# Kernel optimization log

Hardware: AMD Instinct MI355X
Metric: run time of the kernel (lower is better)

Reference implementation:

```python
import jax, jax.numpy as jnp
import numpy as np

B, M, D = 4096, 200, 100          # batch, max_neighbor, embed_dim
NSYM, NENT = 100001, 5000         # num_symbols+1, num_entities


def setup_inputs() -> dict:
    key = jax.random.key(0)
    ks = jax.random.split(key, 12)
    s = 0.05  # weight init scale to keep activations sane
    return {
        "connections": jax.random.randint(ks[0], (B, M, 3), 0, NENT),
        "target": jax.random.randint(ks[1], (B, 1, 2), 0, NENT),
        "symbol_emb": jax.random.normal(ks[2], (NSYM, D), jnp.float32),
        "co_entities": jax.random.uniform(ks[3], (NENT, NENT), dtype=jnp.float32),
        "gcn_w_weight": jax.random.normal(ks[4], (D, 2 * D), jnp.float32) * s,
        "gcn_w_bias": jax.random.normal(ks[5], (D,), jnp.float32) * s,
        "gcn_b": jnp.zeros((D,), jnp.float32),
        "attn_w_weight": jax.random.normal(ks[6], (1, D), jnp.float32) * s,
        "attn_w_bias": jnp.zeros((1,), jnp.float32),
        "gate_w_weight": jax.random.normal(ks[7], (1, D), jnp.float32) * s,
        "gate_w_bias": jnp.zeros((1,), jnp.float32),
        "gate_b": jnp.zeros((1,), jnp.float32),
    }


def reference(connections, target, symbol_emb, co_entities,
              gcn_w_weight, gcn_w_bias, gcn_b,
              attn_w_weight, attn_w_bias,
              gate_w_weight, gate_w_bias, gate_b):
    # --- neighbor gather ---
    relations = connections[:, :, 1]            # [B, M]
    entities = connections[:, :, 2]             # [B, M]
    entself = connections[:, 0, 0]              # [B]
    rel_embeds = symbol_emb[relations]          # [B, M, D]
    ent_embeds = symbol_emb[entities]           # [B, M, D]
    entself_embeds = symbol_emb[entself]        # [B, D]

    # co-occurrence weights: co[b, m] = co_entities[entities[b,m], target_ent[b]]
    target_ent = target[:, 0, 0]                # [B]
    co_weight = co_entities[entities, target_ent[:, None]]  # [B, M]

    # --- linear + leaky_relu (gcn) ---
    concat = jnp.concatenate([rel_embeds, ent_embeds], axis=-1)   # [B, M, 2D]
    out = jnp.einsum('bmk,dk->bmd', concat, gcn_w_weight) + gcn_w_bias + gcn_b
    out = jax.nn.leaky_relu(out, negative_slope=0.01)             # [B, M, D]

    # --- attention over neighbors ---
    attn_out = jnp.einsum('bmd,od->bmo', out, attn_w_weight) + attn_w_bias  # [B, M, 1]
    attn_weight = jax.nn.softmax(attn_out, axis=1)
    out_attn = jnp.einsum('bmd,bmo->bd', out, attn_weight)        # [B, D]

    # --- sigmoid gate ---
    gate = jax.nn.sigmoid(out_attn @ gate_w_weight.T + gate_w_bias + gate_b)  # [B, 1]
    out_neigh = out_attn * gate

    # --- co-weighted neighbor aggregation ---
    neighbor_emb = jnp.einsum('bm,bmd->bd', co_weight, ent_embeds)  # [B, D]

    return out_neigh + entself_embeds * (1.0 - gate) + neighbor_emb
```

## Files before the change

### kernel.cpp

```cpp
#include <hip/hip_runtime.h>

#define BB   4096
#define MM   200
#define DD   100
#define NENT 5000
#define CH   100
#define LPW  30
#define PTW  101

typedef _Float16 f16x2 __attribute__((ext_vector_type(2)));
typedef unsigned uint2v __attribute__((ext_vector_type(2)));

#if defined(__has_builtin)
#if __has_builtin(__builtin_amdgcn_fdot2)
#define HAS_FDOT2 1
#endif
#endif

__device__ __forceinline__ f16x2 uh(unsigned u) { return __builtin_bit_cast(f16x2, u); }
__device__ __forceinline__ float2 h2f(f16x2 h) { return make_float2((float)h.x, (float)h.y); }


__global__ __launch_bounds__(256) void precompute_kernel(
    const float* __restrict__ sym, const float* __restrict__ W,
    const float* __restrict__ wb, const float* __restrict__ gb,
    _Float16* __restrict__ Pr, _Float16* __restrict__ PES)
{
    __shared__ _Float16 Wt[200 * 102];
    const int tid = threadIdx.x;
    for (int j = tid; j < 20000; j += 256) {
        int d = j / 200, k = j % 200;
        Wt[k * 102 + d] = (_Float16)W[j];
    }
    __syncthreads();

    const int i = blockIdx.x * 256 + tid;
    if (i >= NENT * 50) return;
    const int e = i / 50, dp = i % 50;
    const float* se = sym + e * DD;

    float pr0 = 0.f, pr1 = 0.f, pe0 = 0.f, pe1 = 0.f;
    for (int k = 0; k < 100; k++) {
        float a = se[k];
        f16x2 w01 = *(const f16x2*)&Wt[k * 102 + 2 * dp];
        f16x2 w23 = *(const f16x2*)&Wt[(k + 100) * 102 + 2 * dp];
        pr0 = fmaf(a, (float)w01.x, pr0);
        pr1 = fmaf(a, (float)w01.y, pr1);
        pe0 = fmaf(a, (float)w23.x, pe0);
        pe1 = fmaf(a, (float)w23.y, pe1);
    }
    const int d0 = 2 * dp;
    pr0 += wb[d0]     + gb[d0];
    pr1 += wb[d0 + 1] + gb[d0 + 1];

    *(f16x2*)&Pr[e * DD + d0]           = f16x2{(_Float16)pr0, (_Float16)pr1};
    *(f16x2*)&PES[e * 2 * DD + d0]      = f16x2{(_Float16)pe0, (_Float16)pe1};
    *(f16x2*)&PES[e * 2 * DD + DD + d0] = f16x2{(_Float16)se[d0], (_Float16)se[d0 + 1]};
}

__global__ __launch_bounds__(256, 6) void main_kernel(
    const int*  __restrict__ conn, const int* __restrict__ target,
    const float* __restrict__ sym, const float* __restrict__ co,
    const _Float16* __restrict__ Pr, const _Float16* __restrict__ PES,
    const float* __restrict__ attn_w,
    const float* __restrict__ gate_w, const float* __restrict__ gate_wb,
    const float* __restrict__ gate_b,
    float* __restrict__ outp)
{
    __shared__ __align__(16) unsigned char scratch_raw[2 * 10 * PTW * 4];
    __shared__ unsigned idx_s[MM];
    __shared__ float    co_s[MM];
    __shared__ float    ev_s[MM];
    __shared__ float    red[8];
    _Float16* lp_s = (_Float16*)scratch_raw;
    float*    part = (float*)scratch_raw;

    const int t = threadIdx.x;
    const int b = blockIdx.x;
    const int* cb = conn + b * (MM * 3);
    const int lane = t & 63, wid = t >> 6;

    float co_reg = 0.f;
    if (t < MM) {
        int r = cb[t * 3 + 1];
        int e = cb[t * 3 + 2];
        idx_s[t] = (unsigned)r | ((unsigned)e << 16);
        int tgt = target[b * 2];
        co_reg = co[(long)e * NENT + tgt];
    }
    __syncthreads();

    const int g = t / 25, dq = t % 25;
    const bool act = (t < 250);

    float4 awf = *(const float4*)&attn_w[4 * dq];
#ifdef HAS_FDOT2
    f16x2 aw01 = f16x2{(_Float16)awf.x, (_Float16)awf.y};
    f16x2 aw23 = f16x2{(_Float16)awf.z, (_Float16)awf.w};
#endif
    const _Float16 slope = (_Float16)0.01f;

    float oa0 = 0.f, oa1 = 0.f, oa2 = 0.f, oa3 = 0.f;
    f16x2 nb01 = f16x2{(_Float16)0.f, (_Float16)0.f};
    f16x2 nb23 = nb01;
    float gsum = 0.f;

    for (int c = 0; c < 2; ++c) {
        uint2v xs[10];

        if (act) {
            #pragma unroll
            for (int it = 0; it < 10; ++it) {
                int ml = g + 10 * it;
                int m = c * CH + ml;
                unsigned ir = idx_s[m];
                int r = ir & 0xffff, e = ir >> 16;
                uint2v pru = *(const uint2v*)(Pr + r * DD + 4 * dq);
                uint2v peu = *(const uint2v*)(PES + e * 2 * DD + 4 * dq);
                f16x2 x01 = uh(pru.x) + uh(peu.x);
                f16x2 x23 = uh(pru.y) + uh(peu.y);
                x01 = __builtin_elementwise_max(x01, x01 * slope);
                x23 = __builtin_elementwise_max(x23, x23 * slope);
                xs[it].x = __builtin_bit_cast(unsigned, x01);
                xs[it].y = __builtin_bit_cast(unsigned, x23);
                float lp;
#ifdef HAS_FDOT2
                lp = __builtin_amdgcn_fdot2(x01, aw01, 0.0f, false);
                lp = __builtin_amdgcn_fdot2(x23, aw23, lp, false);
#else
                float2 f01 = h2f(x01), f23 = h2f(x23);
                lp = f01.x * awf.x + f01.y * awf.y + f23.x * awf.z + f23.y * awf.w;
#endif
                lp_s[ml * LPW + dq] = (_Float16)lp;
            }
        }
        __syncthreads();

        float ev = 0.f;
        if (t < CH) {
            const _Float16* row = lp_s + t * LPW;
            const unsigned* rw = (const unsigned*)row;
            float acc0 = 0.f, acc1 = 0.f, acc2 = 0.f, acc3 = 0.f;
            #pragma unroll
            for (int i = 0; i < 12; i += 4) {
                float2 a = h2f(uh(rw[i]));
                float2 b2 = h2f(uh(rw[i + 1]));
                float2 cc = h2f(uh(rw[i + 2]));
                float2 d = h2f(uh(rw[i + 3]));
                acc0 += a.x + a.y;
                acc1 += b2.x + b2.y;
                acc2 += cc.x + cc.y;
                acc3 += d.x + d.y;
            }
            float logit = (acc0 + acc1) + (acc2 + acc3) + (float)row[24];
            ev = __expf(logit);
            ev_s[c * CH + t] = ev;
        }
        if (c == 0 && t < MM) co_s[t] = co_reg;
        float s = ev;
        for (int off = 32; off >= 1; off >>= 1) s += __shfl_xor(s, off);
        if (lane == 0) red[4 + wid] = s;
        __syncthreads();
        gsum += (red[4] + red[5]) + (red[6] + red[7]);

        if (act) {
            #pragma unroll
            for (int it = 0; it < 10; ++it) {
                int ml = g + 10 * it;
                int m = c * CH + ml;
                float w = ev_s[m];
                float2 f01 = h2f(uh(xs[it].x));
                float2 f23 = h2f(uh(xs[it].y));
                oa0 = fmaf(w, f01.x, oa0);
                oa1 = fmaf(w, f01.y, oa1);
                oa2 = fmaf(w, f23.x, oa2);
                oa3 = fmaf(w, f23.y, oa3);
                int e = idx_s[m] >> 16;
                uint2v syu = *(const uint2v*)(PES + e * 2 * DD + DD + 4 * dq);
                _Float16 coh = (_Float16)co_s[m];
                f16x2 co2 = f16x2{coh, coh};
                nb01 = co2 * uh(syu.x) + nb01;
                nb23 = co2 * uh(syu.y) + nb23;
            }
        }
    }
    float inv = 1.f / gsum;
    oa0 *= inv; oa1 *= inv; oa2 *= inv; oa3 *= inv;

    if (act) {
        float* po = &part[g * PTW + 4 * dq];
        po[0] = oa0; po[1] = oa1; po[2] = oa2; po[3] = oa3;
        float2 n01 = h2f(nb01), n23 = h2f(nb23);
        float* pn = &part[(10 + g) * PTW + 4 * dq];
        pn[0] = n01.x; pn[1] = n01.y; pn[2] = n23.x; pn[3] = n23.y;
    }
    __syncthreads();

    float oaf = 0.f, nbf = 0.f;
    if (t < DD) {
        #pragma unroll
        for (int g2 = 0; g2 < 10; ++g2) {
            oaf += part[g2 * PTW + t];
            nbf += part[(10 + g2) * PTW + t];
        }
    }

    float p = (t < DD) ? oaf * gate_w[t] : 0.f;
    for (int off = 32; off >= 1; off >>= 1) p += __shfl_xor(p, off);
    if (lane == 0) red[wid] = p;
    __syncthreads();
    float dot = (red[0] + red[1]) + (red[2] + red[3]);
    float gt = 1.f / (1.f + __expf(-(dot + gate_wb[0] + gate_b[0])));

    if (t < DD) {
        float self_v = sym[cb[0] * DD + t];
        outp[b * DD + t] = oaf * gt + self_v * (1.f - gt) + nbf;
    }
}

extern "C" void kernel_launch(void* const* d_in, const int* in_sizes, int n_in,
                              void* d_out, int out_size, void* d_ws, size_t ws_size,
                              hipStream_t stream) {
    const int*   conn    = (const int*)  d_in[0];
    const int*   target  = (const int*)  d_in[1];
    const float* sym     = (const float*)d_in[2];
    const float* co      = (const float*)d_in[3];
    const float* W       = (const float*)d_in[4];
    const float* wb      = (const float*)d_in[5];
    const float* gb      = (const float*)d_in[6];
    const float* attn_w  = (const float*)d_in[7];
    const float* gate_w  = (const float*)d_in[9];
    const float* gate_wb = (const float*)d_in[10];
    const float* gate_b  = (const float*)d_in[11];

    _Float16* Pr  = (_Float16*)d_ws;
    _Float16* PES = (_Float16*)((char*)d_ws + 1000000);

    precompute_kernel<<<(NENT * 50 + 255) / 256, 256, 0, stream>>>(
        sym, W, wb, gb, Pr, PES);

    main_kernel<<<BB, 256, 0, stream>>>(
        conn, target, sym, co, Pr, PES,
        attn_w, gate_w, gate_wb, gate_b, (float*)d_out);
}
```

Measured before the change: 68.99 us.

## Process two batch rows per block with interleaved thread mapping and byte offsets

```diff
diff --git a/kernel.cpp b/kernel.cpp
--- a/kernel.cpp
+++ b/kernel.cpp
@@ -6,7 +6,7 @@
 #define NENT 5000
 #define CH   100
 #define LPW  30
-#define PTW  101
+#define NGR  5
 
 typedef _Float16 f16x2 __attribute__((ext_vector_type(2)));
 typedef unsigned uint2v __attribute__((ext_vector_type(2)));
@@ -58,7 +58,7 @@
     *(f16x2*)&PES[e * 2 * DD + DD + d0] = f16x2{(_Float16)se[d0], (_Float16)se[d0 + 1]};
 }
 
-__global__ __launch_bounds__(256, 6) void main_kernel(
+__global__ __launch_bounds__(256, 4) void main_kernel(
     const int*  __restrict__ conn, const int* __restrict__ target,
     const float* __restrict__ sym, const float* __restrict__ co,
     const _Float16* __restrict__ Pr, const _Float16* __restrict__ PES,
@@ -67,31 +67,45 @@
     const float* __restrict__ gate_b,
     float* __restrict__ outp)
 {
-    __shared__ __align__(16) unsigned char scratch_raw[2 * 10 * PTW * 4];
-    __shared__ unsigned idx_s[MM];
-    __shared__ float    co_s[MM];
-    __shared__ float    ev_s[MM];
-    __shared__ float    red[8];
+    __shared__ __align__(16) unsigned char scratch_raw[12000];
+    __shared__ uint2  off_s[2 * MM];
+    __shared__ float  co_s[2 * MM];
+    __shared__ float  ev_s[2 * CH];
+    __shared__ float  red[8];
+    __shared__ int    s_self[2];
     _Float16* lp_s = (_Float16*)scratch_raw;
     float*    part = (float*)scratch_raw;
 
     const int t = threadIdx.x;
-    const int b = blockIdx.x;
-    const int* cb = conn + b * (MM * 3);
+    const long b0 = 2L * blockIdx.x;
     const int lane = t & 63, wid = t >> 6;
-
-    float co_reg = 0.f;
-    if (t < MM) {
-        int r = cb[t * 3 + 1];
-        int e = cb[t * 3 + 2];
-        idx_s[t] = (unsigned)r | ((unsigned)e << 16);
-        int tgt = target[b * 2];
-        co_reg = co[(long)e * NENT + tgt];
-    }
-    __syncthreads();
-
-    const int g = t / 25, dq = t % 25;
-    const bool act = (t < 250);
+    const int row = t & 1, u = t >> 1;
+
+    float co_r0 = 0.f, co_r1 = 0.f;
+    {
+        int r0w = t & 1, ml0 = t >> 1;
+        const int* cbr = conn + (b0 + r0w) * (MM * 3);
+        int r = cbr[ml0 * 3 + 1];
+        int e = cbr[ml0 * 3 + 2];
+        off_s[t] = make_uint2((unsigned)(r * 200), (unsigned)(e * 400));
+        int tgt = target[(b0 + r0w) * 2];
+        co_r0 = co[(long)e * NENT + tgt];
+        if (t < 144) {
+            int j1 = t + 256;
+            int r1w = j1 & 1, ml1 = j1 >> 1;
+            const int* cbr1 = conn + (b0 + r1w) * (MM * 3);
+            int r1 = cbr1[ml1 * 3 + 1];
+            int e1 = cbr1[ml1 * 3 + 2];
+            off_s[j1] = make_uint2((unsigned)(r1 * 200), (unsigned)(e1 * 400));
+            int tgt1 = target[(b0 + r1w) * 2];
+            co_r1 = co[(long)e1 * NENT + tgt1];
+        }
+        if (t < 2) s_self[t] = conn[(b0 + t) * (MM * 3)];
+    }
+    __syncthreads();
+
+    const int g = u / 25, dq = u % 25;
+    const bool act = (u < NGR * 25);
 
     float4 awf = *(const float4*)&attn_w[4 * dq];
 #ifdef HAS_FDOT2
@@ -106,17 +120,17 @@
     float gsum = 0.f;
 
     for (int c = 0; c < 2; ++c) {
-        uint2v xs[10];
+        uint2v xs[20];
 
         if (act) {
             #pragma unroll
-            for (int it = 0; it < 10; ++it) {
-                int ml = g + 10 * it;
-                int m = c * CH + ml;
-                unsigned ir = idx_s[m];
-                int r = ir & 0xffff, e = ir >> 16;
-                uint2v pru = *(const uint2v*)(Pr + r * DD + 4 * dq);
-                uint2v peu = *(const uint2v*)(PES + e * 2 * DD + 4 * dq);
+            for (int it = 0; it < 20; ++it) {
+                int lm = g + NGR * it;
+                uint2 off = off_s[(c * CH + lm) * 2 + row];
+                const char* prp = (const char*)Pr + off.x + (dq << 3);
+                const char* pep = (const char*)PES + off.y + (dq << 3);
+                uint2v pru = *(const uint2v*)prp;
+                uint2v peu = *(const uint2v*)pep;
                 f16x2 x01 = uh(pru.x) + uh(peu.x);
                 f16x2 x23 = uh(pru.y) + uh(peu.y);
                 x01 = __builtin_elementwise_max(x01, x01 * slope);
@@ -131,15 +145,15 @@
                 float2 f01 = h2f(x01), f23 = h2f(x23);
                 lp = f01.x * awf.x + f01.y * awf.y + f23.x * awf.z + f23.y * awf.w;
 #endif
-                lp_s[ml * LPW + dq] = (_Float16)lp;
+                lp_s[(lm * 2 + row) * LPW + dq] = (_Float16)lp;
             }
         }
         __syncthreads();
 
         float ev = 0.f;
-        if (t < CH) {
-            const _Float16* row = lp_s + t * LPW;
-            const unsigned* rw = (const unsigned*)row;
+        if (t < 2 * CH) {
+            const _Float16* rowp = lp_s + t * LPW;
+            const unsigned* rw = (const unsigned*)rowp;
             float acc0 = 0.f, acc1 = 0.f, acc2 = 0.f, acc3 = 0.f;
             #pragma unroll
             for (int i = 0; i < 12; i += 4) {
@@ -152,32 +166,39 @@
                 acc2 += cc.x + cc.y;
                 acc3 += d.x + d.y;
             }
-            float logit = (acc0 + acc1) + (acc2 + acc3) + (float)row[24];
+            float logit = (acc0 + acc1) + (acc2 + acc3) + (float)rowp[24];
             ev = __expf(logit);
-            ev_s[c * CH + t] = ev;
-        }
-        if (c == 0 && t < MM) co_s[t] = co_reg;
+            ev_s[t] = ev;
+        }
+        if (c == 0) {
+            co_s[t] = co_r0;
+            if (t < 144) co_s[t + 256] = co_r1;
+        }
         float s = ev;
-        for (int off = 32; off >= 1; off >>= 1) s += __shfl_xor(s, off);
-        if (lane == 0) red[4 + wid] = s;
+        s += __shfl_xor(s, 32);
+        s += __shfl_xor(s, 16);
+        s += __shfl_xor(s, 8);
+        s += __shfl_xor(s, 4);
+        s += __shfl_xor(s, 2);
+        if ((lane >> 1) == 0) red[wid * 2 + (lane & 1)] = s;
         __syncthreads();
-        gsum += (red[4] + red[5]) + (red[6] + red[7]);
+        gsum += ((red[0 + row] + red[2 + row]) + (red[4 + row] + red[6 + row]));
 
         if (act) {
             #pragma unroll
-            for (int it = 0; it < 10; ++it) {
-                int ml = g + 10 * it;
-                int m = c * CH + ml;
-                float w = ev_s[m];
+            for (int it = 0; it < 20; ++it) {
+                int lm = g + NGR * it;
+                float w = ev_s[lm * 2 + row];
                 float2 f01 = h2f(uh(xs[it].x));
                 float2 f23 = h2f(uh(xs[it].y));
                 oa0 = fmaf(w, f01.x, oa0);
                 oa1 = fmaf(w, f01.y, oa1);
                 oa2 = fmaf(w, f23.x, oa2);
                 oa3 = fmaf(w, f23.y, oa3);
-                int e = idx_s[m] >> 16;
-                uint2v syu = *(const uint2v*)(PES + e * 2 * DD + DD + 4 * dq);
-                _Float16 coh = (_Float16)co_s[m];
+                uint2 off = off_s[(c * CH + lm) * 2 + row];
+                const char* pep = (const char*)PES + off.y + (dq << 3);
+                uint2v syu = *(const uint2v*)(pep + 200);
+                _Float16 coh = (_Float16)co_s[(c * CH + lm) * 2 + row];
                 f16x2 co2 = f16x2{coh, coh};
                 nb01 = co2 * uh(syu.x) + nb01;
                 nb23 = co2 * uh(syu.y) + nb23;
@@ -188,33 +209,38 @@
     oa0 *= inv; oa1 *= inv; oa2 *= inv; oa3 *= inv;
 
     if (act) {
-        float* po = &part[g * PTW + 4 * dq];
+        float* po = &part[((0 * 2 + row) * NGR + g) * DD + 4 * dq];
         po[0] = oa0; po[1] = oa1; po[2] = oa2; po[3] = oa3;
         float2 n01 = h2f(nb01), n23 = h2f(nb23);
-        float* pn = &part[(10 + g) * PTW + 4 * dq];
+        float* pn = &part[((1 * 2 + row) * NGR + g) * DD + 4 * dq];
         pn[0] = n01.x; pn[1] = n01.y; pn[2] = n23.x; pn[3] = n23.y;
     }
     __syncthreads();
 
     float oaf = 0.f, nbf = 0.f;
-    if (t < DD) {
+    const int d = u;
+    if (t < 2 * DD) {
         #pragma unroll
-        for (int g2 = 0; g2 < 10; ++g2) {
-            oaf += part[g2 * PTW + t];
-            nbf += part[(10 + g2) * PTW + t];
-        }
-    }
-
-    float p = (t < DD) ? oaf * gate_w[t] : 0.f;
-    for (int off = 32; off >= 1; off >>= 1) p += __shfl_xor(p, off);
-    if (lane == 0) red[wid] = p;
-    __syncthreads();
-    float dot = (red[0] + red[1]) + (red[2] + red[3]);
+        for (int g2 = 0; g2 < NGR; ++g2) {
+            oaf += part[((0 * 2 + row) * NGR + g2) * DD + d];
+            nbf += part[((1 * 2 + row) * NGR + g2) * DD + d];
+        }
+    }
+
+    float p = (t < 2 * DD) ? oaf * gate_w[d] : 0.f;
+    p += __shfl_xor(p, 32);
+    p += __shfl_xor(p, 16);
+    p += __shfl_xor(p, 8);
+    p += __shfl_xor(p, 4);
+    p += __shfl_xor(p, 2);
+    if ((lane >> 1) == 0) red[wid * 2 + (lane & 1)] = p;
+    __syncthreads();
+    float dot = ((red[0 + row] + red[2 + row]) + (red[4 + row] + red[6 + row]));
     float gt = 1.f / (1.f + __expf(-(dot + gate_wb[0] + gate_b[0])));
 
-    if (t < DD) {
-        float self_v = sym[cb[0] * DD + t];
-        outp[b * DD + t] = oaf * gt + self_v * (1.f - gt) + nbf;
+    if (t < 2 * DD) {
+        float self_v = sym[(long)s_self[row] * DD + d];
+        outp[(b0 + row) * DD + d] = oaf * gt + self_v * (1.f - gt) + nbf;
     }
 }
 
@@ -239,7 +265,7 @@
     precompute_kernel<<<(NENT * 50 + 255) / 256, 256, 0, stream>>>(
         sym, W, wb, gb, Pr, PES);
 
-    main_kernel<<<BB, 256, 0, stream>>>(
+    main_kernel<<<BB / 2, 256, 0, stream>>>(
         conn, target, sym, co, Pr, PES,
         attn_w, gate_w, gate_wb, gate_b, (float*)d_out);
 }
```

Result: slower. 148.2 us (+114.9%).

## Split neighbor dimension across blocks with a second reduction kernel

Applied to the files above, without the earlier changes.

```diff
diff --git a/kernel.cpp b/kernel.cpp
--- a/kernel.cpp
+++ b/kernel.cpp
@@ -4,9 +4,8 @@
 #define MM   200
 #define DD   100
 #define NENT 5000
-#define CH   100
 #define LPW  30
-#define PTW  101
+#define PSTR 204
 
 typedef _Float16 f16x2 __attribute__((ext_vector_type(2)));
 typedef unsigned uint2v __attribute__((ext_vector_type(2)));
@@ -58,163 +57,186 @@
     *(f16x2*)&PES[e * 2 * DD + DD + d0] = f16x2{(_Float16)se[d0], (_Float16)se[d0 + 1]};
 }
 
-__global__ __launch_bounds__(256, 6) void main_kernel(
+template<int MPB>
+__global__ __launch_bounds__(256, 6) void b1_kernel(
     const int*  __restrict__ conn, const int* __restrict__ target,
-    const float* __restrict__ sym, const float* __restrict__ co,
+    const float* __restrict__ co,
     const _Float16* __restrict__ Pr, const _Float16* __restrict__ PES,
     const float* __restrict__ attn_w,
+    float* __restrict__ part_ws)
+{
+    constexpr int NS    = MM / MPB;
+    constexpr int ITERS = MPB / 10;
+    constexpr int SCR   = (MPB * 2 * LPW > 8080) ? MPB * 2 * LPW : 8080;
+    __shared__ __align__(16) unsigned char scratch_raw[SCR];
+    __shared__ unsigned idx_s[MPB];
+    __shared__ float    co_s[MPB];
+    __shared__ float    ev_s[MPB];
+    __shared__ float    red[4];
+    _Float16* lp_s = (_Float16*)scratch_raw;
+    float*    part = (float*)scratch_raw;
+
+    const int t = threadIdx.x;
+    const int bid = blockIdx.x;
+    const int row = bid / NS, seg = bid % NS;
+    const int* cb = conn + row * (MM * 3) + seg * (MPB * 3);
+    const int lane = t & 63, wid = t >> 6;
+
+    float co_reg = 0.f;
+    if (t < MPB) {
+        int r = cb[t * 3 + 1];
+        int e = cb[t * 3 + 2];
+        idx_s[t] = (unsigned)r | ((unsigned)e << 16);
+        int tgt = target[row * 2];
+        co_reg = co[(long)e * NENT + tgt];
+    }
+    __syncthreads();
+
+    const int g = t / 25, dq = t % 25;
+    const bool act = (t < 250);
+
+    float4 awf = *(const float4*)&attn_w[4 * dq];
+#ifdef HAS_FDOT2
+    f16x2 aw01 = f16x2{(_Float16)awf.x, (_Float16)awf.y};
+    f16x2 aw23 = f16x2{(_Float16)awf.z, (_Float16)awf.w};
+#endif
+    const _Float16 slope = (_Float16)0.01f;
+
+    uint2v xs[ITERS];
+
+    if (act) {
+        #pragma unroll
+        for (int it = 0; it < ITERS; ++it) {
+            int lm = g + 10 * it;
+            unsigned ir = idx_s[lm];
+            int r = ir & 0xffff, e = ir >> 16;
+            uint2v pru = *(const uint2v*)(Pr + r * DD + 4 * dq);
+            uint2v peu = *(const uint2v*)(PES + e * 2 * DD + 4 * dq);
+            f16x2 x01 = uh(pru.x) + uh(peu.x);
+            f16x2 x23 = uh(pru.y) + uh(peu.y);
+            x01 = __builtin_elementwise_max(x01, x01 * slope);
+            x23 = __builtin_elementwise_max(x23, x23 * slope);
+            xs[it].x = __builtin_bit_cast(unsigned, x01);
+            xs[it].y = __builtin_bit_cast(unsigned, x23);
+            float lp;
+#ifdef HAS_FDOT2
+            lp = __builtin_amdgcn_fdot2(x01, aw01, 0.0f, false);
+            lp = __builtin_amdgcn_fdot2(x23, aw23, lp, false);
+#else
+            float2 f01 = h2f(x01), f23 = h2f(x23);
+            lp = f01.x * awf.x + f01.y * awf.y + f23.x * awf.z + f23.y * awf.w;
+#endif
+            lp_s[lm * LPW + dq] = (_Float16)lp;
+        }
+    }
+    __syncthreads();
+
+    float ev = 0.f;
+    if (t < MPB) {
+        const _Float16* rowp = lp_s + t * LPW;
+        const unsigned* rw = (const unsigned*)rowp;
+        float acc0 = 0.f, acc1 = 0.f, acc2 = 0.f, acc3 = 0.f;
+        #pragma unroll
+        for (int i = 0; i < 12; i += 4) {
+            float2 a = h2f(uh(rw[i]));
+            float2 b2 = h2f(uh(rw[i + 1]));
+            float2 cc = h2f(uh(rw[i + 2]));
+            float2 d = h2f(uh(rw[i + 3]));
+            acc0 += a.x + a.y;
+            acc1 += b2.x + b2.y;
+            acc2 += cc.x + cc.y;
+            acc3 += d.x + d.y;
+        }
+        float logit = (acc0 + acc1) + (acc2 + acc3) + (float)rowp[24];
+        ev = __expf(logit);
+        ev_s[t] = ev;
+        co_s[t] = co_reg;
+    }
+    float s = ev;
+    for (int off = 32; off >= 1; off >>= 1) s += __shfl_xor(s, off);
+    if (lane == 0) red[wid] = s;
+    __syncthreads();
+    const float gsum = (red[0] + red[1]) + (red[2] + red[3]);
+
+    float oa0 = 0.f, oa1 = 0.f, oa2 = 0.f, oa3 = 0.f;
+    f16x2 nb01 = f16x2{(_Float16)0.f, (_Float16)0.f};
+    f16x2 nb23 = nb01;
+    if (act) {
+        #pragma unroll
+        for (int it = 0; it < ITERS; ++it) {
+            int lm = g + 10 * it;
+            float w = ev_s[lm];
+            float2 f01 = h2f(uh(xs[it].x));
+            float2 f23 = h2f(uh(xs[it].y));
+            oa0 = fmaf(w, f01.x, oa0);
+            oa1 = fmaf(w, f01.y, oa1);
+            oa2 = fmaf(w, f23.x, oa2);
+            oa3 = fmaf(w, f23.y, oa3);
+            int e = idx_s[lm] >> 16;
+            uint2v syu = *(const uint2v*)(PES + e * 2 * DD + DD + 4 * dq);
+            _Float16 coh = (_Float16)co_s[lm];
+            f16x2 co2 = f16x2{coh, coh};
+            nb01 = co2 * uh(syu.x) + nb01;
+            nb23 = co2 * uh(syu.y) + nb23;
+        }
+    }
+
+    if (act) {
+        float* po = &part[g * 101 + 4 * dq];
+        po[0] = oa0; po[1] = oa1; po[2] = oa2; po[3] = oa3;
+        float2 n01 = h2f(nb01), n23 = h2f(nb23);
+        float* pn = &part[(10 + g) * 101 + 4 * dq];
+        pn[0] = n01.x; pn[1] = n01.y; pn[2] = n23.x; pn[3] = n23.y;
+    }
+    __syncthreads();
+
+    if (t < DD) {
+        float oap = 0.f, nbp = 0.f;
+        #pragma unroll
+        for (int g2 = 0; g2 < 10; ++g2) {
+            oap += part[g2 * 101 + t];
+            nbp += part[(10 + g2) * 101 + t];
+        }
+        float* po = part_ws + (long)bid * PSTR;
+        po[t] = oap;
+        po[DD + t] = nbp;
+    }
+    if (t == 0) part_ws[(long)bid * PSTR + 2 * DD] = gsum;
+}
+
+__global__ __launch_bounds__(128) void b2_kernel(
+    const float* __restrict__ part_ws, int ns,
+    const int* __restrict__ conn, const float* __restrict__ sym,
     const float* __restrict__ gate_w, const float* __restrict__ gate_wb,
     const float* __restrict__ gate_b,
     float* __restrict__ outp)
 {
-    __shared__ __align__(16) unsigned char scratch_raw[2 * 10 * PTW * 4];
-    __shared__ unsigned idx_s[MM];
-    __shared__ float    co_s[MM];
-    __shared__ float    ev_s[MM];
-    __shared__ float    red[8];
-    _Float16* lp_s = (_Float16*)scratch_raw;
-    float*    part = (float*)scratch_raw;
-
-    const int t = threadIdx.x;
-    const int b = blockIdx.x;
-    const int* cb = conn + b * (MM * 3);
+    __shared__ float red[2];
+    const int r = blockIdx.x, t = threadIdx.x;
     const int lane = t & 63, wid = t >> 6;
 
-    float co_reg = 0.f;
-    if (t < MM) {
-        int r = cb[t * 3 + 1];
-        int e = cb[t * 3 + 2];
-        idx_s[t] = (unsigned)r | ((unsigned)e << 16);
-        int tgt = target[b * 2];
-        co_reg = co[(long)e * NENT + tgt];
-    }
-    __syncthreads();
-
-    const int g = t / 25, dq = t % 25;
-    const bool act = (t < 250);
-
-    float4 awf = *(const float4*)&attn_w[4 * dq];
-#ifdef HAS_FDOT2
-    f16x2 aw01 = f16x2{(_Float16)awf.x, (_Float16)awf.y};
-    f16x2 aw23 = f16x2{(_Float16)awf.z, (_Float16)awf.w};
-#endif
-    const _Float16 slope = (_Float16)0.01f;
-
-    float oa0 = 0.f, oa1 = 0.f, oa2 = 0.f, oa3 = 0.f;
-    f16x2 nb01 = f16x2{(_Float16)0.f, (_Float16)0.f};
-    f16x2 nb23 = nb01;
-    float gsum = 0.f;
-
-    for (int c = 0; c < 2; ++c) {
-        uint2v xs[10];
-
-        if (act) {
-            #pragma unroll
-            for (int it = 0; it < 10; ++it) {
-                int ml = g + 10 * it;
-                int m = c * CH + ml;
-                unsigned ir = idx_s[m];
-                int r = ir & 0xffff, e = ir >> 16;
-                uint2v pru = *(const uint2v*)(Pr + r * DD + 4 * dq);
-                uint2v peu = *(const uint2v*)(PES + e * 2 * DD + 4 * dq);
-                f16x2 x01 = uh(pru.x) + uh(peu.x);
-                f16x2 x23 = uh(pru.y) + uh(peu.y);
-                x01 = __builtin_elementwise_max(x01, x01 * slope);
-                x23 = __builtin_elementwise_max(x23, x23 * slope);
-                xs[it].x = __builtin_bit_cast(unsigned, x01);
-                xs[it].y = __builtin_bit_cast(unsigned, x23);
-                float lp;
-#ifdef HAS_FDOT2
-                lp = __builtin_amdgcn_fdot2(x01, aw01, 0.0f, false);
-                lp = __builtin_amdgcn_fdot2(x23, aw23, lp, false);
-#else
-                float2 f01 = h2f(x01), f23 = h2f(x23);
-                lp = f01.x * awf.x + f01.y * awf.y + f23.x * awf.z + f23.y * awf.w;
-#endif
-                lp_s[ml * LPW + dq] = (_Float16)lp;
-            }
-        }
-        __syncthreads();
-
-        float ev = 0.f;
-        if (t < CH) {
-            const _Float16* row = lp_s + t * LPW;
-            const unsigned* rw = (const unsigned*)row;
-            float acc0 = 0.f, acc1 = 0.f, acc2 = 0.f, acc3 = 0.f;
-            #pragma unroll
-            for (int i = 0; i < 12; i += 4) {
-                float2 a = h2f(uh(rw[i]));
-                float2 b2 = h2f(uh(rw[i + 1]));
-                float2 cc = h2f(uh(rw[i + 2]));
-                float2 d = h2f(uh(rw[i + 3]));
-                acc0 += a.x + a.y;
-                acc1 += b2.x + b2.y;
-                acc2 += cc.x + cc.y;
-                acc3 += d.x + d.y;
-            }
-            float logit = (acc0 + acc1) + (acc2 + acc3) + (float)row[24];
-            ev = __expf(logit);
-            ev_s[c * CH + t] = ev;
-        }
-        if (c == 0 && t < MM) co_s[t] = co_reg;
-        float s = ev;
-        for (int off = 32; off >= 1; off >>= 1) s += __shfl_xor(s, off);
-        if (lane == 0) red[4 + wid] = s;
-        __syncthreads();
-        gsum += (red[4] + red[5]) + (red[6] + red[7]);
-
-        if (act) {
-            #pragma unroll
-            for (int it = 0; it < 10; ++it) {
-                int ml = g + 10 * it;
-                int m = c * CH + ml;
-                float w = ev_s[m];
-                float2 f01 = h2f(uh(xs[it].x));
-                float2 f23 = h2f(uh(xs[it].y));
-                oa0 = fmaf(w, f01.x, oa0);
-                oa1 = fmaf(w, f01.y, oa1);
-                oa2 = fmaf(w, f23.x, oa2);
-                oa3 = fmaf(w, f23.y, oa3);
-                int e = idx_s[m] >> 16;
-                uint2v syu = *(const uint2v*)(PES + e * 2 * DD + DD + 4 * dq);
-                _Float16 coh = (_Float16)co_s[m];
-                f16x2 co2 = f16x2{coh, coh};
-                nb01 = co2 * uh(syu.x) + nb01;
-                nb23 = co2 * uh(syu.y) + nb23;
-            }
-        }
-    }
-    float inv = 1.f / gsum;
-    oa0 *= inv; oa1 *= inv; oa2 *= inv; oa3 *= inv;
-
-    if (act) {
-        float* po = &part[g * PTW + 4 * dq];
-        po[0] = oa0; po[1] = oa1; po[2] = oa2; po[3] = oa3;
-        float2 n01 = h2f(nb01), n23 = h2f(nb23);
-        float* pn = &part[(10 + g) * PTW + 4 * dq];
-        pn[0] = n01.x; pn[1] = n01.y; pn[2] = n23.x; pn[3] = n23.y;
-    }
-    __syncthreads();
-
-    float oaf = 0.f, nbf = 0.f;
-    if (t < DD) {
-        #pragma unroll
-        for (int g2 = 0; g2 < 10; ++g2) {
-            oaf += part[g2 * PTW + t];
-            nbf += part[(10 + g2) * PTW + t];
-        }
-    }
+    float oaf = 0.f, nbf = 0.f, gs = 0.f;
+    const float* base = part_ws + (long)r * ns * PSTR;
+    for (int s2 = 0; s2 < ns; ++s2) {
+        gs += base[s2 * PSTR + 2 * DD];
+        if (t < DD) {
+            oaf += base[s2 * PSTR + t];
+            nbf += base[s2 * PSTR + DD + t];
+        }
+    }
+    oaf /= gs;
 
     float p = (t < DD) ? oaf * gate_w[t] : 0.f;
     for (int off = 32; off >= 1; off >>= 1) p += __shfl_xor(p, off);
     if (lane == 0) red[wid] = p;
     __syncthreads();
-    float dot = (red[0] + red[1]) + (red[2] + red[3]);
+    float dot = red[0] + red[1];
     float gt = 1.f / (1.f + __expf(-(dot + gate_wb[0] + gate_b[0])));
 
     if (t < DD) {
-        float self_v = sym[cb[0] * DD + t];
-        outp[b * DD + t] = oaf * gt + self_v * (1.f - gt) + nbf;
+        int s_self = conn[(long)r * (MM * 3)];
+        float self_v = sym[(long)s_self * DD + t];
+        outp[(long)r * DD + t] = oaf * gt + self_v * (1.f - gt) + nbf;
     }
 }
 
@@ -235,11 +257,27 @@
 
     _Float16* Pr  = (_Float16*)d_ws;
     _Float16* PES = (_Float16*)((char*)d_ws + 1000000);
+    float* part_ws = (float*)((char*)d_ws + 3000000);
+
+    const size_t basev = 3000000;
+    int ns = 4;
+    if (ws_size < basev + (size_t)BB * 4 * PSTR * 4) ns = 2;
+    if (ws_size < basev + (size_t)BB * 2 * PSTR * 4) ns = 1;
 
     precompute_kernel<<<(NENT * 50 + 255) / 256, 256, 0, stream>>>(
         sym, W, wb, gb, Pr, PES);
 
-    main_kernel<<<BB, 256, 0, stream>>>(
-        conn, target, sym, co, Pr, PES,
-        attn_w, gate_w, gate_wb, gate_b, (float*)d_out);
-}
+    if (ns == 4) {
+        b1_kernel<50><<<BB * 4, 256, 0, stream>>>(
+            conn, target, co, Pr, PES, attn_w, part_ws);
+    } else if (ns == 2) {
+        b1_kernel<100><<<BB * 2, 256, 0, stream>>>(
+            conn, target, co, Pr, PES, attn_w, part_ws);
+    } else {
+        b1_kernel<200><<<BB, 256, 0, stream>>>(
+            conn, target, co, Pr, PES, attn_w, part_ws);
+    }
+
+    b2_kernel<<<BB, 128, 0, stream>>>(
+        part_ws, ns, conn, sym, gate_w, gate_wb, gate_b, (float*)d_out);
+}
```

After: 71.86 us. +4.2%, slower.
